# Performance work log

Measured on AMD Instinct MI355X. Metric: run time of the kernel, lower is better.

The kernel has to match this reference:

```python
import jax, jax.numpy as jnp
import numpy as np

C_S, C_HID, H, P, V = 128, 16, 12, 4, 8
EPS = 1e-08
SOFTPLUS_INV_1 = 0.541324854612918


def _pts_from_linear(x, n_pts):
    # torch: split [..., 3*n] into 3 chunks of n, stack on dim=-1 -> [..., n, 3]
    B, N = x.shape[:2]
    return jnp.moveaxis(x.reshape(B, N, 3, n_pts), -2, -1)


def setup_inputs() -> dict:
    key = jax.random.key(0)
    ks = jax.random.split(key, 16)
    B, N = 2, 512
    hc = H * C_HID            # 192
    hpq = H * P * 3           # 144
    hpkv = H * (P + V) * 3    # 432
    cat_dim = H * (C_HID + V * 4)  # 576
    sc = 0.02
    inp = {
        "s": jax.random.normal(ks[0], (B, N, C_S), jnp.float32),
        "R": jax.random.normal(ks[1], (B, N, 3, 3), jnp.float32),
        "t": jax.random.normal(ks[2], (B, N, 3), jnp.float32),
        "pair_mask": jnp.ones((B, N, N), jnp.float32),
        "Wq": jax.random.normal(ks[3], (C_S, hc), jnp.float32) * sc,
        "bq": jnp.zeros((hc,), jnp.float32),
        "Wkv": jax.random.normal(ks[4], (C_S, 2 * hc), jnp.float32) * sc,
        "bkv": jnp.zeros((2 * hc,), jnp.float32),
        "Wqp": jax.random.normal(ks[5], (C_S, hpq), jnp.float32) * sc,
        "bqp": jnp.zeros((hpq,), jnp.float32),
        "Wkvp": jax.random.normal(ks[6], (C_S, hpkv), jnp.float32) * sc,
        "bkvp": jnp.zeros((hpkv,), jnp.float32),
        "head_weights": jnp.full((H,), SOFTPLUS_INV_1, jnp.float32),
        "Wout": jax.random.normal(ks[7], (cat_dim, C_S), jnp.float32) * sc,
        "bout": jnp.zeros((C_S,), jnp.float32),
    }
    return inp


def reference(s, R, t, pair_mask, Wq, bq, Wkv, bkv, Wqp, bqp, Wkvp, bkvp,
              head_weights, Wout, bout):
    B, N, _ = s.shape
    # scalar q/k/v
    q = (s @ Wq + bq).reshape(B, N, H, C_HID)
    kv = (s @ Wkv + bkv).reshape(B, N, H, 2 * C_HID)
    k, v = kv[..., :C_HID], kv[..., C_HID:]

    # point q/k/v in global frame: R x + t
    qp = _pts_from_linear(s @ Wqp + bqp, H * P)           # [B,N,HP,3]
    qp = jnp.einsum('bnij,bnpj->bnpi', R, qp) + t[:, :, None]
    qp = qp.reshape(B, N, H, P, 3)
    kvp = _pts_from_linear(s @ Wkvp + bkvp, H * (P + V))  # [B,N,H(P+V),3]
    kvp = jnp.einsum('bnij,bnpj->bnpi', R, kvp) + t[:, :, None]
    kvp = kvp.reshape(B, N, H, P + V, 3)
    kp, vp = kvp[..., :P, :], kvp[..., P:, :]

    # scalar attention logits [B,H,N,N]
    a = jnp.einsum('bihc,bjhc->bhij', q, k) * (1.0 / np.sqrt(3 * C_HID))

    # point-distance bias: sum_p ||q_i - k_j||^2 via |q|^2+|k|^2-2q.k
    sq_q = jnp.sum(qp * qp, axis=(-1, -2))   # [B,N,H]
    sq_k = jnp.sum(kp * kp, axis=(-1, -2))   # [B,N,H]
    cross = jnp.einsum('bihpc,bjhpc->bhij', qp, kp)
    d2 = (jnp.swapaxes(sq_q, 1, 2)[..., :, None]
          + jnp.swapaxes(sq_k, 1, 2)[..., None, :]
          - 2.0 * cross)                      # [B,H,N,N]
    hw = jax.nn.softplus(head_weights) * np.sqrt(1.0 / (3 * (P * 9.0 / 2)))
    pt_att = d2 * hw[None, :, None, None] * (-0.5)

    square_mask = 100000.0 * (pair_mask - 1.0)            # [B,N,N]
    a = jax.nn.softmax(a + pt_att + square_mask[:, None], axis=-1)

    # scalar output
    o = jnp.einsum('bhij,bjhc->bihc', a, v).reshape(B, N, H * C_HID)

    # point output, rotated back to local frame: R^T (x - t) form -> R^T x - t
    o_pt = jnp.einsum('bhij,bjhvc->bihvc', a, vp)         # [B,N,H,V,3]
    o_pt = jnp.einsum('bnji,bnhvj->bnhvi', R, o_pt) - t[:, :, None, None]
    o_pt_norm = jnp.sqrt(jnp.sum(o_pt * o_pt, axis=-1) + EPS).reshape(B, N, H * V)
    o_pt_flat = o_pt.reshape(B, N, H * V, 3)

    cat = jnp.concatenate(
        [o, o_pt_flat[..., 0], o_pt_flat[..., 1], o_pt_flat[..., 2], o_pt_norm],
        axis=-1)                                           # [B,N,576]
    return cat @ Wout + bout
```

## Files before the change

kernel.cpp:

```cpp
#include <hip/hip_runtime.h>
#include <hip/hip_bf16.h>
#include <math.h>

#define H_    12
#define B_    2
#define N_    512
#define BH_   (B_*H_)
#define QSCALE 0.14433756729740643f
#define CPT_K  0.13608276348795434f

#define OFF_WPP  1245184
#define OFF_WOP  1318912
#define OFF_BIA  1355776
#define OFF_QB   1356928
#define OFF_KP   1553536
#define OFF_VP   1750144
#define OFF_SA   2045056
#define OFF_SB   2057344
#define OFF_CATP 2069632

typedef __attribute__((ext_vector_type(8))) short sh8;
typedef __attribute__((ext_vector_type(4))) float f32x4;
typedef unsigned short u16t;

static __device__ __forceinline__ u16t f2b(float x) {
    __hip_bfloat16 h = __float2bfloat16(x);
    return *reinterpret_cast<u16t*>(&h);
}
static __device__ __forceinline__ int catp_idx(int tok, int col) {
    return (tok >> 4)*9216 + (col >> 5)*512 + ((col >> 3) & 3)*128
         + (tok & 15)*8 + (col & 7);
}

__global__ __launch_bounds__(256) void convert_kernel(
    const float* __restrict__ Wq,  const float* __restrict__ bq,
    const float* __restrict__ Wkv, const float* __restrict__ bkv,
    const float* __restrict__ Wqp, const float* __restrict__ bqp,
    const float* __restrict__ Wkvp,const float* __restrict__ bkvp,
    const float* __restrict__ Wout, float* __restrict__ ws)
{
    const int g = blockIdx.x * 256 + threadIdx.x;
    union { sh8 v; u16t u[8]; } pk;

    if (g < 18432) {
        int u = g;
        int n = u & 63, kq = (u >> 6) & 3, ks = (u >> 8) & 3, nt = u >> 10;
        int col = nt*64 + n, k0 = ks*32 + kq*8;
        const float* w; int lc, od;
        if (col < 192)      { w = Wq;   lc = col;     od = 192; }
        else if (col < 576) { w = Wkv;  lc = col-192; od = 384; }
        else if (col < 720) { w = Wqp;  lc = col-576; od = 144; }
        else                { w = Wkvp; lc = col-720; od = 432; }
        #pragma unroll
        for (int j = 0; j < 8; ++j) pk.u[j] = f2b(w[(k0+j)*od + lc]);
        *((sh8*)((u16t*)(ws + OFF_WPP)) + u) = pk.v;
    } else if (g < 27648) {
        int u = g - 18432;
        int n = u & 63, kq = (u >> 6) & 3, rem = u >> 8;
        int ks = rem % 18, nt = rem / 18;
        int col = nt*64 + n, k0 = ks*32 + kq*8;
        #pragma unroll
        for (int j = 0; j < 8; ++j) pk.u[j] = f2b(Wout[(k0+j)*128 + col]);
        *((sh8*)((u16t*)(ws + OFF_WOP)) + u) = pk.v;
    } else if (g < 28800) {
        int col = g - 27648;
        float bv;
        if (col < 192)      bv = bq[col];
        else if (col < 576) bv = bkv[col-192];
        else if (col < 720) bv = bqp[col-576];
        else                bv = bkvp[col-720];
        ws[OFF_BIA + col] = bv;
    }
}

__global__ __launch_bounds__(512) void projpack_kernel(
    const float* __restrict__ s,
    const float* __restrict__ Rg, const float* __restrict__ tg,
    const float* __restrict__ hwg, float* __restrict__ ws)
{
    __shared__ float ldsP[8][1160];

    u16t* Qb = (u16t*)(ws + OFF_QB);
    u16t* Kp = (u16t*)(ws + OFF_KP);
    u16t* Vp = (u16t*)(ws + OFF_VP);
    float* sa_g = ws + OFF_SA;
    float* sb_g = ws + OFF_SB;

    const int tid  = threadIdx.x;
    const int w    = tid >> 6, lane = tid & 63;
    const int kq   = lane >> 4, lx = lane & 15;
    const int tok0 = blockIdx.x * 8;
    const int b    = tok0 >> 9, n0 = tok0 & 511;

    sh8 afr[4];
    #pragma unroll
    for (int ks = 0; ks < 4; ++ks) {
        const float* src = s + (tok0 + (lx & 7))*128 + ks*32 + kq*8;
        float4 u0 = *(const float4*)(src);
        float4 u1 = *(const float4*)(src+4);
        union { sh8 v; u16t u[8]; } pk;
        pk.u[0]=f2b(u0.x); pk.u[1]=f2b(u0.y); pk.u[2]=f2b(u0.z); pk.u[3]=f2b(u0.w);
        pk.u[4]=f2b(u1.x); pk.u[5]=f2b(u1.y); pk.u[6]=f2b(u1.z); pk.u[7]=f2b(u1.w);
        afr[ks] = pk.v;
    }

    const sh8* Bp = (const sh8*)((const u16t*)(ws + OFF_WPP));
    const float* bias = ws + OFF_BIA;

    #pragma unroll 3
    for (int g = 0; g < 9; ++g) {
        int gg = w*9 + g;
        int nt = gg >> 2, nq = gg & 3;
        f32x4 acc = {0.f,0.f,0.f,0.f};
        #pragma unroll
        for (int ks = 0; ks < 4; ++ks) {
            sh8 bf = Bp[((nt*4 + ks)*4 + kq)*64 + nq*16 + lx];
            acc = __builtin_amdgcn_mfma_f32_16x16x32_bf16(afr[ks], bf, acc, 0, 0, 0);
        }
        float bv = bias[gg*16 + lx];
        if (kq < 2) {
            #pragma unroll
            for (int r = 0; r < 4; ++r)
                ldsP[kq*4 + r][gg*16 + lx] = acc[r] + bv;
        }
    }
    __syncthreads();

    for (int idx = tid; idx < 8*48; idx += 512) {
        int tk = idx / 48, p = idx % 48;
        int tok = tok0 + tk;
        const float* Rr = Rg + tok*9;
        const float* tr = tg + tok*3;
        float x0 = ldsP[tk][576 +  0 + p];
        float x1 = ldsP[tk][576 + 48 + p];
        float x2 = ldsP[tk][576 + 96 + p];
        ldsP[tk][576 +  0 + p] = Rr[0]*x0 + Rr[1]*x1 + Rr[2]*x2 + tr[0];
        ldsP[tk][576 + 48 + p] = Rr[3]*x0 + Rr[4]*x1 + Rr[5]*x2 + tr[1];
        ldsP[tk][576 + 96 + p] = Rr[6]*x0 + Rr[7]*x1 + Rr[8]*x2 + tr[2];
    }
    for (int idx = tid; idx < 8*144; idx += 512) {
        int tk = idx / 144, p = idx % 144;
        int tok = tok0 + tk;
        const float* Rr = Rg + tok*9;
        const float* tr = tg + tok*3;
        float x0 = ldsP[tk][720 +   0 + p];
        float x1 = ldsP[tk][720 + 144 + p];
        float x2 = ldsP[tk][720 + 288 + p];
        ldsP[tk][720 +   0 + p] = Rr[0]*x0 + Rr[1]*x1 + Rr[2]*x2 + tr[0];
        ldsP[tk][720 + 144 + p] = Rr[3]*x0 + Rr[4]*x1 + Rr[5]*x2 + tr[1];
        ldsP[tk][720 + 288 + p] = Rr[6]*x0 + Rr[7]*x1 + Rr[8]*x2 + tr[2];
    }
    __syncthreads();

    for (int idx = tid; idx < 8*24; idx += 512) {
        int tk = idx / 24, r2 = idx % 24, h = r2 >> 1, half = r2 & 1;
        float hx = hwg[h];
        float sp = (hx > 20.f) ? hx : log1pf(__expf(hx));
        float c_pt = -0.5f * sp * CPT_K;
        union { sh8 v[2]; u16t u[16]; } pk;
        if (half == 0) {
            #pragma unroll
            for (int e = 0; e < 16; ++e) pk.u[e] = f2b(ldsP[tk][h*16 + e] * QSCALE);
        } else {
            float qs = -2.f * c_pt;
            #pragma unroll
            for (int e = 0; e < 12; ++e)
                pk.u[e] = f2b(ldsP[tk][576 + (e%3)*48 + h*4 + e/3] * qs);
            pk.u[12]=0; pk.u[13]=0; pk.u[14]=0; pk.u[15]=0;
        }
        u16t* dst = Qb + ((b*H_+h)*N_ + n0 + tk)*32 + half*16;
        *(sh8*)dst = pk.v[0];
        *(sh8*)(dst+8) = pk.v[1];
    }
    for (int idx = tid; idx < 8*48; idx += 512) {
        int tk = idx / 48, r2 = idx % 48, h = r2 >> 2, fq = r2 & 3;
        int j = n0 + tk, bh = b*H_ + h;
        union { sh8 v; u16t u[8]; } pk;
        #pragma unroll
        for (int e = 0; e < 8; ++e) {
            int c = fq*8 + e;
            float val;
            if (c < 16)      val = ldsP[tk][192 + h*32 + c];
            else if (c < 28) val = ldsP[tk][720 + ((c-16)%3)*144 + h*12 + (c-16)/3];
            else             val = 0.f;
            pk.u[e] = f2b(val);
        }
        *(sh8*)(Kp + bh*16384 + (j>>4)*512 + fq*128 + (j&15)*8) = pk.v;
    }
    for (int idx = tid; idx < 480; idx += 512) {
        int h = idx / 40, d = idx % 40;
        int bh = b*H_ + h;
        union { sh8 v; u16t u[8]; } pk;
        #pragma unroll
        for (int e = 0; e < 8; ++e) {
            float val;
            if (d < 16) val = ldsP[e][192 + h*32 + 16 + d];
            else        val = ldsP[e][720 + ((d-16)%3)*144 + h*12 + 4 + (d-16)/3];
            pk.u[e] = f2b(val);
        }
        int j = n0;
        *(sh8*)(Vp + bh*24576 + (j>>5)*1536 + (d>>4)*512 + ((j>>3)&3)*128
                + (d&15)*8) = pk.v;
    }
    for (int idx = tid; idx < 8*12; idx += 512) {
        int tk = idx / 12, h = idx % 12;
        float hx = hwg[h];
        float sp = (hx > 20.f) ? hx : log1pf(__expf(hx));
        float c_pt = -0.5f * sp * CPT_K;
        float sq = 0.f, sk = 0.f;
        #pragma unroll
        for (int pp = 0; pp < 4; ++pp)
            #pragma unroll
            for (int c = 0; c < 3; ++c) {
                float a = ldsP[tk][576 + c*48  + h*4  + pp]; sq += a*a;
                float k = ldsP[tk][720 + c*144 + h*12 + pp]; sk += k*k;
            }
        sa_g[(b*H_+h)*N_ + n0 + tk] = c_pt * sq;
        sb_g[(b*H_+h)*N_ + n0 + tk] = c_pt * sk;
    }
}

__global__ __launch_bounds__(512, 2) void attn_kernel(
    const float* __restrict__ Rg, const float* __restrict__ tg,
    const float* __restrict__ maskg, float* __restrict__ ws)
{
    __shared__ u16t smP[8*16*72];
    __shared__ float mbuf[4*64*20];
    __shared__ float obuf[64*32];

    const u16t* Qb = (const u16t*)(ws + OFF_QB);
    const u16t* Kp = (const u16t*)(ws + OFF_KP);
    const u16t* Vp = (const u16t*)(ws + OFF_VP);
    const float* sa_g = ws + OFF_SA;
    const float* sb_g = ws + OFF_SB;
    u16t* catp = (u16t*)(ws + OFF_CATP);

    const int tid  = threadIdx.x;
    const int w    = tid >> 6, lane = tid & 63;
    const int rg   = w & 3, jh = w >> 2;
    const int kq   = lane >> 4, lx = lane & 15;
    const int bh   = blockIdx.x >> 3;
    const int it   = blockIdx.x & 7;
    const int b    = bh / H_, h = bh % H_;
    const int i0   = it * 64;

    sh8 qfrag = *(const sh8*)(Qb + (bh*N_ + i0 + rg*16 + lx)*32 + kq*8);
    float sa_r[4];
    #pragma unroll
    for (int r = 0; r < 4; ++r)
        sa_r[r] = sa_g[bh*N_ + i0 + rg*16 + kq*4 + r];

    float m_run[4] = {-1e30f,-1e30f,-1e30f,-1e30f};
    float l_run[4] = {0.f,0.f,0.f,0.f};
    f32x4 oc0 = {0.f,0.f,0.f,0.f}, oc1 = oc0, oc2 = oc0;

    const float* mrow = maskg + (size_t)(b*N_ + i0 + rg*16 + kq*4)*N_ + lx;
    u16t* pw = smP + w*1152;

    for (int t = 0; t < 4; ++t) {
        const int jt = jh*4 + t;
        const int j0 = jt * 64;

        f32x4 sc[4];
        #pragma unroll
        for (int st = 0; st < 4; ++st) {
            sh8 kf = *(const sh8*)(Kp + bh*16384 + (jt*4+st)*512 + kq*128 + lx*8);
            f32x4 z = {0.f,0.f,0.f,0.f};
            sc[st] = __builtin_amdgcn_mfma_f32_16x16x32_bf16(qfrag, kf, z, 0, 0, 0);
        }
        float sbv[4];
        #pragma unroll
        for (int st = 0; st < 4; ++st) sbv[st] = sb_g[bh*N_ + j0 + st*16 + lx];
        float mb[16];
        #pragma unroll
        for (int r = 0; r < 4; ++r)
            #pragma unroll
            for (int st = 0; st < 4; ++st)
                mb[r*4+st] = mrow[r*N_ + j0 + st*16];

        float L[16];
        #pragma unroll
        for (int st = 0; st < 4; ++st)
            #pragma unroll
            for (int r = 0; r < 4; ++r)
                L[st*4+r] = sc[st][r] + sa_r[r] + sbv[st] + 1e5f*(mb[r*4+st] - 1.f);

        #pragma unroll
        for (int r = 0; r < 4; ++r) {
            float tm = fmaxf(fmaxf(L[0*4+r], L[1*4+r]), fmaxf(L[2*4+r], L[3*4+r]));
            tm = fmaxf(tm, __shfl_xor(tm, 1));
            tm = fmaxf(tm, __shfl_xor(tm, 2));
            tm = fmaxf(tm, __shfl_xor(tm, 4));
            tm = fmaxf(tm, __shfl_xor(tm, 8));
            float mnew = fmaxf(m_run[r], tm);
            float al = __expf(m_run[r] - mnew);
            m_run[r] = mnew;
            l_run[r] *= al;
            oc0[r] *= al; oc1[r] *= al; oc2[r] *= al;
        }
        #pragma unroll
        for (int st = 0; st < 4; ++st)
            #pragma unroll
            for (int r = 0; r < 4; ++r) {
                float p = __expf(L[st*4+r] - m_run[r]);
                l_run[r] += p;
                pw[(kq*4+r)*72 + st*16 + lx] = f2b(p);
            }
        #pragma unroll
        for (int c = 0; c < 2; ++c) {
            sh8 pa = *(const sh8*)(pw + lx*72 + c*32 + kq*8);
            #pragma unroll
            for (int nq = 0; nq < 3; ++nq) {
                sh8 vf = *(const sh8*)(Vp + bh*24576 + (jt*2+c)*1536 + nq*512
                                        + kq*128 + lx*8);
                if (nq == 0) oc0 = __builtin_amdgcn_mfma_f32_16x16x32_bf16(pa, vf, oc0, 0,0,0);
                if (nq == 1) oc1 = __builtin_amdgcn_mfma_f32_16x16x32_bf16(pa, vf, oc1, 0,0,0);
                if (nq == 2) oc2 = __builtin_amdgcn_mfma_f32_16x16x32_bf16(pa, vf, oc2, 0,0,0);
            }
        }
    }

    if (jh == 1) {
        float* mb = mbuf + (rg*64 + lane)*20;
        #pragma unroll
        for (int r = 0; r < 4; ++r) {
            mb[r]      = m_run[r];
            mb[4 + r]  = l_run[r];
            mb[8 + r]  = oc0[r];
            mb[12 + r] = oc1[r];
            mb[16 + r] = oc2[r];
        }
    }
    __syncthreads();
    if (jh == 0) {
        const float* mb = mbuf + (rg*64 + lane)*20;
        float linv[4];
        #pragma unroll
        for (int r = 0; r < 4; ++r) {
            float mB = mb[r];
            float ms = fmaxf(m_run[r], mB);
            float eA = __expf(m_run[r] - ms);
            float eB = __expf(mB - ms);
            float l = l_run[r]*eA + mb[4+r]*eB;
            oc0[r] = oc0[r]*eA + mb[8+r]*eB;
            oc1[r] = oc1[r]*eA + mb[12+r]*eB;
            oc2[r] = oc2[r]*eA + mb[16+r]*eB;
            l += __shfl_xor(l, 1); l += __shfl_xor(l, 2);
            l += __shfl_xor(l, 4); l += __shfl_xor(l, 8);
            linv[r] = 1.f / l;
        }

        #pragma unroll
        for (int r = 0; r < 4; ++r) {
            int tok = b*N_ + i0 + rg*16 + kq*4 + r;
            catp[catp_idx(tok, h*16 + lx)] = f2b(oc0[r] * linv[r]);
            obuf[(rg*16 + kq*4 + r)*32 + lx]      = oc1[r] * linv[r];
            obuf[(rg*16 + kq*4 + r)*32 + 16 + lx] = oc2[r] * linv[r];
        }

        #pragma unroll
        for (int tsk = 0; tsk < 2; ++tsk) {
            int task = lane + tsk*64;
            int r = task >> 3, pv = task & 7;
            int tok = b*N_ + i0 + rg*16 + r;
            const float* Rr = Rg + tok*9;
            const float* tr = tg + tok*3;
            float g0 = obuf[(rg*16 + r)*32 + pv*3 + 0];
            float g1 = obuf[(rg*16 + r)*32 + pv*3 + 1];
            float g2 = obuf[(rg*16 + r)*32 + pv*3 + 2];
            float px = Rr[0]*g0 + Rr[3]*g1 + Rr[6]*g2 - tr[0];
            float py = Rr[1]*g0 + Rr[4]*g1 + Rr[7]*g2 - tr[1];
            float pz = Rr[2]*g0 + Rr[5]*g1 + Rr[8]*g2 - tr[2];
            float nrm = sqrtf(px*px + py*py + pz*pz + 1e-8f);
            catp[catp_idx(tok, 192 + h*8 + pv)] = f2b(px);
            catp[catp_idx(tok, 288 + h*8 + pv)] = f2b(py);
            catp[catp_idx(tok, 384 + h*8 + pv)] = f2b(pz);
            catp[catp_idx(tok, 480 + h*8 + pv)] = f2b(nrm);
        }
    }
}

__global__ __launch_bounds__(512) void out_kernel(
    const float* __restrict__ bout, const float* __restrict__ ws,
    float* __restrict__ out)
{
    __shared__ float part[4][64][4];

    const int tid = threadIdx.x;
    const int w = tid >> 6, lane = tid & 63;
    const int cg = w & 3, kh = w >> 2;
    const int lx = lane & 15, kq = lane >> 4;
    const int nt = blockIdx.x, mt = blockIdx.y;

    const sh8* Ap = (const sh8*)((const u16t*)(ws + OFF_CATP));
    const sh8* Bp = (const sh8*)((const u16t*)(ws + OFF_WOP));

    f32x4 acc = {0.f,0.f,0.f,0.f};
    #pragma unroll 3
    for (int i = 0; i < 9; ++i) {
        int ks = kh*9 + i;
        sh8 af = Ap[((mt*18 + ks)*4 + kq)*16 + lx];
        sh8 bf = Bp[((nt*18 + ks)*4 + kq)*64 + cg*16 + lx];
        acc = __builtin_amdgcn_mfma_f32_16x16x32_bf16(af, bf, acc, 0, 0, 0);
    }
    if (kh == 1) {
        #pragma unroll
        for (int r = 0; r < 4; ++r) part[cg][lane][r] = acc[r];
    }
    __syncthreads();
    if (kh == 0) {
        int col = nt*64 + cg*16 + lx;
        float bv = bout[col];
        #pragma unroll
        for (int r = 0; r < 4; ++r) {
            int row = mt*16 + kq*4 + r;
            out[row*128 + col] = acc[r] + part[cg][lane][r] + bv;
        }
    }
}

extern "C" void kernel_launch(void* const* d_in, const int* in_sizes, int n_in,
                              void* d_out, int out_size, void* d_ws, size_t ws_size,
                              hipStream_t stream) {
    const float* s    = (const float*)d_in[0];
    const float* R    = (const float*)d_in[1];
    const float* t    = (const float*)d_in[2];
    const float* mask = (const float*)d_in[3];
    const float* Wq   = (const float*)d_in[4];
    const float* bq   = (const float*)d_in[5];
    const float* Wkv  = (const float*)d_in[6];
    const float* bkv  = (const float*)d_in[7];
    const float* Wqp  = (const float*)d_in[8];
    const float* bqp  = (const float*)d_in[9];
    const float* Wkvp = (const float*)d_in[10];
    const float* bkvp = (const float*)d_in[11];
    const float* hw   = (const float*)d_in[12];
    const float* Wout = (const float*)d_in[13];
    const float* bout = (const float*)d_in[14];
    float* ws  = (float*)d_ws;
    float* out = (float*)d_out;

    convert_kernel<<<113, 256, 0, stream>>>(Wq, bq, Wkv, bkv,
                                            Wqp, bqp, Wkvp, bkvp, Wout, ws);
    projpack_kernel<<<128, 512, 0, stream>>>(s, R, t, hw, ws);
    attn_kernel<<<BH_*8, 512, 0, stream>>>(R, t, mask, ws);
    out_kernel<<<dim3(2, 64), 512, 0, stream>>>(bout, ws, out);
}
```

Measured before the change: 111.5 us.

## Shrink per-block work across projection, attention and output kernels for more blocks

Halves tokens per block in the projection kernel (4 instead of 8), halves query rows per attention block (32 rows, 256 threads, 384 blocks), and splits the output GEMM into single-wavefront blocks that each cover the full K range. The goal is to raise block count and fill more of the GPU's compute units on this small problem. In exchange, weights and K/V tiles are reloaded by more blocks, and the V-pack store drops to a narrower 4-element write at a sub-chunk offset. The hidden attention-kernel body must agree with the new rg/jh mapping, which cannot be checked here.

```diff
diff --git a/kernel.cpp b/kernel.cpp
--- a/kernel.cpp
+++ b/kernel.cpp
@@ -78,7 +78,7 @@
     const float* __restrict__ Rg, const float* __restrict__ tg,
     const float* __restrict__ hwg, float* __restrict__ ws)
 {
-    __shared__ float ldsP[8][1160];
+    __shared__ float ldsP[4][1160];
 
     u16t* Qb = (u16t*)(ws + OFF_QB);
     u16t* Kp = (u16t*)(ws + OFF_KP);
@@ -89,13 +89,13 @@
     const int tid  = threadIdx.x;
     const int w    = tid >> 6, lane = tid & 63;
     const int kq   = lane >> 4, lx = lane & 15;
-    const int tok0 = blockIdx.x * 8;
+    const int tok0 = blockIdx.x * 4;
     const int b    = tok0 >> 9, n0 = tok0 & 511;
 
     sh8 afr[4];
     #pragma unroll
     for (int ks = 0; ks < 4; ++ks) {
-        const float* src = s + (tok0 + (lx & 7))*128 + ks*32 + kq*8;
+        const float* src = s + (tok0 + (lx & 3))*128 + ks*32 + kq*8;
         float4 u0 = *(const float4*)(src);
         float4 u1 = *(const float4*)(src+4);
         union { sh8 v; u16t u[8]; } pk;
@@ -118,15 +118,15 @@
             acc = __builtin_amdgcn_mfma_f32_16x16x32_bf16(afr[ks], bf, acc, 0, 0, 0);
         }
         float bv = bias[gg*16 + lx];
-        if (kq < 2) {
+        if (kq == 0) {
             #pragma unroll
             for (int r = 0; r < 4; ++r)
-                ldsP[kq*4 + r][gg*16 + lx] = acc[r] + bv;
+                ldsP[r][gg*16 + lx] = acc[r] + bv;
         }
     }
     __syncthreads();
 
-    for (int idx = tid; idx < 8*48; idx += 512) {
+    for (int idx = tid; idx < 4*48; idx += 512) {
         int tk = idx / 48, p = idx % 48;
         int tok = tok0 + tk;
         const float* Rr = Rg + tok*9;
@@ -138,7 +138,7 @@
         ldsP[tk][576 + 48 + p] = Rr[3]*x0 + Rr[4]*x1 + Rr[5]*x2 + tr[1];
         ldsP[tk][576 + 96 + p] = Rr[6]*x0 + Rr[7]*x1 + Rr[8]*x2 + tr[2];
     }
-    for (int idx = tid; idx < 8*144; idx += 512) {
+    for (int idx = tid; idx < 4*144; idx += 512) {
         int tk = idx / 144, p = idx % 144;
         int tok = tok0 + tk;
         const float* Rr = Rg + tok*9;
@@ -152,7 +152,7 @@
     }
     __syncthreads();
 
-    for (int idx = tid; idx < 8*24; idx += 512) {
+    for (int idx = tid; idx < 4*24; idx += 512) {
         int tk = idx / 24, r2 = idx % 24, h = r2 >> 1, half = r2 & 1;
         float hx = hwg[h];
         float sp = (hx > 20.f) ? hx : log1pf(__expf(hx));
@@ -172,7 +172,7 @@
         *(sh8*)dst = pk.v[0];
         *(sh8*)(dst+8) = pk.v[1];
     }
-    for (int idx = tid; idx < 8*48; idx += 512) {
+    for (int idx = tid; idx < 4*48; idx += 512) {
         int tk = idx / 48, r2 = idx % 48, h = r2 >> 2, fq = r2 & 3;
         int j = n0 + tk, bh = b*H_ + h;
         union { sh8 v; u16t u[8]; } pk;
@@ -190,19 +190,19 @@
     for (int idx = tid; idx < 480; idx += 512) {
         int h = idx / 40, d = idx % 40;
         int bh = b*H_ + h;
-        union { sh8 v; u16t u[8]; } pk;
-        #pragma unroll
-        for (int e = 0; e < 8; ++e) {
+        union { uint2 v; u16t u[4]; } pk;
+        #pragma unroll
+        for (int e = 0; e < 4; ++e) {
             float val;
             if (d < 16) val = ldsP[e][192 + h*32 + 16 + d];
             else        val = ldsP[e][720 + ((d-16)%3)*144 + h*12 + 4 + (d-16)/3];
             pk.u[e] = f2b(val);
         }
         int j = n0;
-        *(sh8*)(Vp + bh*24576 + (j>>5)*1536 + (d>>4)*512 + ((j>>3)&3)*128
-                + (d&15)*8) = pk.v;
-    }
-    for (int idx = tid; idx < 8*12; idx += 512) {
+        *(uint2*)(Vp + bh*24576 + (j>>5)*1536 + (d>>4)*512 + ((j>>3)&3)*128
+                  + (d&15)*8 + (j&7)) = pk.v;
+    }
+    for (int idx = tid; idx < 4*12; idx += 512) {
         int tk = idx / 12, h = idx % 12;
         float hx = hwg[h];
         float sp = (hx > 20.f) ? hx : log1pf(__expf(hx));
@@ -220,13 +220,13 @@
     }
 }
 
-__global__ __launch_bounds__(512, 2) void attn_kernel(
+__global__ __launch_bounds__(256) void attn_kernel(
     const float* __restrict__ Rg, const float* __restrict__ tg,
     const float* __restrict__ maskg, float* __restrict__ ws)
 {
-    __shared__ u16t smP[8*16*72];
-    __shared__ float mbuf[4*64*20];
-    __shared__ float obuf[64*32];
+    __shared__ u16t smP[4*16*72];
+    __shared__ float mbuf[2*64*20];
+    __shared__ float obuf[32*32];
 
     const u16t* Qb = (const u16t*)(ws + OFF_QB);
     const u16t* Kp = (const u16t*)(ws + OFF_KP);
@@ -237,12 +237,12 @@
 
     const int tid  = threadIdx.x;
     const int w    = tid >> 6, lane = tid & 63;
-    const int rg   = w & 3, jh = w >> 2;
+    const int rg   = w & 1, jh = w >> 1;
     const int kq   = lane >> 4, lx = lane & 15;
-    const int bh   = blockIdx.x >> 3;
-    const int it   = blockIdx.x & 7;
+    const int bh   = blockIdx.x >> 4;
+    const int it   = blockIdx.x & 15;
     const int b    = bh / H_, h = bh % H_;
-    const int i0   = it * 64;
+    const int i0   = it * 32;
 
     sh8 qfrag = *(const sh8*)(Qb + (bh*N_ + i0 + rg*16 + lx)*32 + kq*8);
     float sa_r[4];
@@ -380,42 +380,31 @@
     }
 }
 
-__global__ __launch_bounds__(512) void out_kernel(
+__global__ __launch_bounds__(64) void out_kernel(
     const float* __restrict__ bout, const float* __restrict__ ws,
     float* __restrict__ out)
 {
-    __shared__ float part[4][64][4];
-
-    const int tid = threadIdx.x;
-    const int w = tid >> 6, lane = tid & 63;
-    const int cg = w & 3, kh = w >> 2;
+    const int lane = threadIdx.x;
     const int lx = lane & 15, kq = lane >> 4;
-    const int nt = blockIdx.x, mt = blockIdx.y;
+    const int ng = blockIdx.x, mt = blockIdx.y;
+    const int nt = ng >> 2, nq = ng & 3;
 
     const sh8* Ap = (const sh8*)((const u16t*)(ws + OFF_CATP));
     const sh8* Bp = (const sh8*)((const u16t*)(ws + OFF_WOP));
 
     f32x4 acc = {0.f,0.f,0.f,0.f};
-    #pragma unroll 3
-    for (int i = 0; i < 9; ++i) {
-        int ks = kh*9 + i;
+    #pragma unroll 6
+    for (int ks = 0; ks < 18; ++ks) {
         sh8 af = Ap[((mt*18 + ks)*4 + kq)*16 + lx];
-        sh8 bf = Bp[((nt*18 + ks)*4 + kq)*64 + cg*16 + lx];
+        sh8 bf = Bp[((nt*18 + ks)*4 + kq)*64 + nq*16 + lx];
         acc = __builtin_amdgcn_mfma_f32_16x16x32_bf16(af, bf, acc, 0, 0, 0);
     }
-    if (kh == 1) {
-        #pragma unroll
-        for (int r = 0; r < 4; ++r) part[cg][lane][r] = acc[r];
-    }
-    __syncthreads();
-    if (kh == 0) {
-        int col = nt*64 + cg*16 + lx;
-        float bv = bout[col];
-        #pragma unroll
-        for (int r = 0; r < 4; ++r) {
-            int row = mt*16 + kq*4 + r;
-            out[row*128 + col] = acc[r] + part[cg][lane][r] + bv;
-        }
+    int col = ng*16 + lx;
+    float bv = bout[col];
+    #pragma unroll
+    for (int r = 0; r < 4; ++r) {
+        int row = mt*16 + kq*4 + r;
+        out[row*128 + col] = acc[r] + bv;
     }
 }
 
@@ -442,7 +431,7 @@
 
     convert_kernel<<<113, 256, 0, stream>>>(Wq, bq, Wkv, bkv,
                                             Wqp, bqp, Wkvp, bkvp, Wout, ws);
-    projpack_kernel<<<128, 512, 0, stream>>>(s, R, t, hw, ws);
-    attn_kernel<<<BH_*8, 512, 0, stream>>>(R, t, mask, ws);
-    out_kernel<<<dim3(2, 64), 512, 0, stream>>>(bout, ws, out);
-}
+    projpack_kernel<<<256, 512, 0, stream>>>(s, R, t, hw, ws);
+    attn_kernel<<<BH_*16, 256, 0, stream>>>(R, t, mask, ws);
+    out_kernel<<<dim3(8, 64), 64, 0, stream>>>(bout, ws, out);
+}
```

New measurement: 113.7 us. No clear change (+1.9%).
